# Kernel optimization log

Measured on AMD Instinct MI355X. Metric: run time of the kernel, lower is better.

The kernel has to match this reference:

```python
import jax, jax.numpy as jnp
import numpy as np

NEG_SLOPE = 0.01  # nn.LeakyReLU default


def setup_inputs() -> dict:
    key = jax.random.key(0)
    k1, k2, k3, k4, k5, k6 = jax.random.split(key, 6)
    N, E, F_IN, F_OUT = 50000, 800000, 256, 64
    x = jax.random.normal(k1, (N, F_IN), dtype=jnp.float32)
    src = jax.random.randint(k2, (E,), 0, N, dtype=jnp.int32)
    dst = jax.random.randint(k3, (E,), 0, N, dtype=jnp.int32)
    # nn.init.normal_(weight, 0, 0.5) for both Linear layers (no bias)
    W1 = 0.5 * jax.random.normal(k4, (F_OUT, F_IN), dtype=jnp.float32)
    W2 = 0.5 * jax.random.normal(k5, (F_OUT, F_OUT), dtype=jnp.float32)
    # detGAT.a = torch.rand(2*out_feats, 1)
    a = jax.random.uniform(k6, (2 * F_OUT, 1), dtype=jnp.float32)
    return {"x": x, "W1": W1, "W2": W2, "a": a, "src": src, "dst": dst}


def reference(x, W1, W2, a, src, dst):
    N, d = x.shape[0], W1.shape[0]
    # model_base: linear -> (dropout, identity in eval) -> relu, twice
    z = jax.nn.relu(x @ W1.T)
    h = jax.nn.relu(z @ W2.T)  # [N, d]
    # detGAT edge score: LeakyReLU(concat([h_dst, h_src]) @ a)
    # split a so we compute per-node dot products once instead of an [E, 2d] concat
    a_dst, a_src = a[:d, 0], a[d:, 0]
    s_dst = h @ a_dst  # [N]
    s_src = h @ a_src  # [N]
    score = jax.nn.leaky_relu(s_dst[dst] + s_src[src], NEG_SLOPE)  # [E]
    # edge_softmax: softmax over incoming edges of each destination node
    m = jax.ops.segment_max(score, dst, num_segments=N)  # [N]
    e = jnp.exp(score - m[dst])
    ssum = jax.ops.segment_sum(e, dst, num_segments=N)  # [N]
    w = e / ssum[dst]  # [E]
    # weighted scatter-sum of src features to dst nodes
    res = jax.ops.segment_sum(h[src] * w[:, None], dst, num_segments=N)  # [N, d]
    return jax.nn.relu(h - res)
```

## Files before the change

### kernel.cpp

```cpp
#include <hip/hip_runtime.h>
#include <math.h>

#define F_IN 256
#define F_OUT 64
#define NEG_SLOPE 0.01f
#define CAP 8192
#define NB2 256

typedef unsigned short ushort8_t __attribute__((ext_vector_type(8)));
typedef __bf16 bf16x8 __attribute__((ext_vector_type(8)));
typedef float f32x16 __attribute__((ext_vector_type(16)));

__device__ inline unsigned short f2bf(float f) {
    unsigned u = __float_as_uint(f);
    u += 0x7FFF + ((u >> 16) & 1);
    return (unsigned short)(u >> 16);
}
__device__ inline float bf2f(unsigned short u) {
    return __uint_as_float(((unsigned)u) << 16);
}
__device__ inline void splitbf(float x, unsigned short& hi, unsigned short& lo) {
    hi = f2bf(x);
    lo = f2bf(x - bf2f(hi));
}
__device__ inline bf16x8 asbf8(ushort8_t u) {
    union { ushort8_t u; bf16x8 b; } c; c.u = u; return c.b;
}
__device__ inline void split8u(const float4& p0, const float4& p1, ushort8_t& h, ushort8_t& l) {
    unsigned short th, tl;
    splitbf(p0.x, th, tl); h[0] = th; l[0] = tl;
    splitbf(p0.y, th, tl); h[1] = th; l[1] = tl;
    splitbf(p0.z, th, tl); h[2] = th; l[2] = tl;
    splitbf(p0.w, th, tl); h[3] = th; l[3] = tl;
    splitbf(p1.x, th, tl); h[4] = th; l[4] = tl;
    splitbf(p1.y, th, tl); h[5] = th; l[5] = tl;
    splitbf(p1.z, th, tl); h[6] = th; l[6] = tl;
    splitbf(p1.w, th, tl); h[7] = th; l[7] = tl;
}
__device__ inline float redq32(float v) {
    v += __shfl_xor(v, 1);  v += __shfl_xor(v, 2);  v += __shfl_xor(v, 4);
    v += __shfl_xor(v, 8);  v += __shfl_xor(v, 16);
    return v;
}

__global__ __launch_bounds__(1024)
void prep_scatter_kernel(const float* __restrict__ W1, const float* __restrict__ W2,
                         unsigned short* __restrict__ w1fh, unsigned short* __restrict__ w1fl,
                         unsigned short* __restrict__ w2fh, unsigned short* __restrict__ w2fl,
                         const float* __restrict__ x,
                         unsigned short* __restrict__ xfh, unsigned short* __restrict__ xfl,
                         int NTT, int N,
                         const int* __restrict__ src, const int* __restrict__ dst,
                         int* __restrict__ cursor, int* __restrict__ edata,
                         int E, int chunk)
{
    __shared__ int lh[256], lbase[256], lcur[256];
    const int tid = threadIdx.x;

    if (blockIdx.x < 16) {
        int idx = blockIdx.x * 1024 + tid;
        int jj = idx & 7, l = (idx >> 3) & 63, t = idx >> 9;
        {
            int nt = t & 1, gks = t >> 1;
            int f = nt * 32 + (l & 31);
            int k = gks * 16 + (l >> 5) * 8 + jj;
            unsigned short hi, lo;
            splitbf(W1[f * F_IN + k], hi, lo);
            w1fh[idx] = hi; w1fl[idx] = lo;
        }
        if (idx < 4096) {
            int nt = t & 1, ks = t >> 1;
            int f = nt * 32 + (l & 31);
            int j = ks * 16 + (l >> 5) * 8 + jj;
            unsigned short hi, lo;
            splitbf(W2[f * F_OUT + j], hi, lo);
            w2fh[idx] = hi; w2fl[idx] = lo;
        }
        return;
    }

    if (blockIdx.x < 16 + NTT) {
        const int t = blockIdx.x - 16;
        const int gks = tid >> 6, lane = tid & 63;
        const int ml = lane & 31, q = lane >> 5;
        const int row = min(t * 32 + ml, N - 1);
        const float* xr = x + (size_t)row * F_IN + gks * 16 + q * 8;
        float4 p0 = *(const float4*)xr;
        float4 p1 = *(const float4*)(xr + 4);
        ushort8_t h, l;
        split8u(p0, p1, h, l);
        size_t off = ((size_t)t * 1024 + tid) * 8;
        *(ushort8_t*)(xfh + off) = h;
        *(ushort8_t*)(xfl + off) = l;
        return;
    }

    const int bid = blockIdx.x - 16 - NTT;
    if (tid < 256) lh[tid] = 0;
    __syncthreads();
    const int beg = bid * chunk;
    const int end = min(E, beg + chunk);
    for (int i = beg + tid; i < end; i += 1024)
        atomicAdd(&lh[((unsigned)dst[i]) >> 8], 1);
    __syncthreads();
    if (tid < 256) {
        int c = lh[tid];
        lbase[tid] = c ? atomicAdd(&cursor[tid], c) : 0;
        lcur[tid] = 0;
    }
    __syncthreads();
    for (int i = beg + tid; i < end; i += 1024) {
        int d = dst[i];
        int s = src[i];
        int b = ((unsigned)d) >> 8;
        int rk = atomicAdd(&lcur[b], 1);
        edata[b * CAP + lbase[b] + rk] = ((d & 0xFF) << 16) | s;
    }
}

__global__ __launch_bounds__(256, 2)
void mlp_sort_kernel(const unsigned short* __restrict__ xfh,
                     const unsigned short* __restrict__ xfl,
                     const unsigned short* __restrict__ w1fh,
                     const unsigned short* __restrict__ w1fl,
                     const unsigned short* __restrict__ w2fh,
                     const unsigned short* __restrict__ w2fl,
                     const float* __restrict__ a,
                     unsigned short* __restrict__ hb,
                     float* __restrict__ sdst,
                     float* __restrict__ ssrc, int N,
                     const int* __restrict__ cursor,
                     const int* __restrict__ edata,
                     int* __restrict__ ssorted,
                     int* __restrict__ cnt, int* __restrict__ offs,
                     int MLPB)
{
    __shared__ __align__(16) unsigned short zbuf[4 * 4224];
    __shared__ int hist[256];
    __shared__ int excl[256];

    const int tid = threadIdx.x;
    const int lane = tid & 63;

    if (blockIdx.x < MLPB) {
        const int wid = __builtin_amdgcn_readfirstlane(tid >> 6);
        const int ml = lane & 31;
        const int q = lane >> 5;
        const int node0w = blockIdx.x * 128 + wid * 32;
        const int t = blockIdx.x * 4 + wid;

        unsigned short* zh = zbuf + wid * 4224;
        unsigned short* zl = zh + 2112;

        const unsigned short* __restrict__ xbh = xfh + (size_t)t * 8192;
        const unsigned short* __restrict__ xbl = xfl + (size_t)t * 8192;

        f32x16 acc0, acc1;
#pragma unroll
        for (int i = 0; i < 16; i++) { acc0[i] = 0.f; acc1[i] = 0.f; }

#pragma unroll
        for (int gks = 0; gks < 16; gks++) {
            bf16x8 ah = asbf8(*(const ushort8_t*)(xbh + gks * 512 + lane * 8));
            bf16x8 al = asbf8(*(const ushort8_t*)(xbl + gks * 512 + lane * 8));
            bf16x8 bh0 = asbf8(*(const ushort8_t*)(w1fh + ((gks * 2 + 0) * 64 + lane) * 8));
            bf16x8 bl0 = asbf8(*(const ushort8_t*)(w1fl + ((gks * 2 + 0) * 64 + lane) * 8));
            bf16x8 bh1 = asbf8(*(const ushort8_t*)(w1fh + ((gks * 2 + 1) * 64 + lane) * 8));
            bf16x8 bl1 = asbf8(*(const ushort8_t*)(w1fl + ((gks * 2 + 1) * 64 + lane) * 8));
            acc0 = __builtin_amdgcn_mfma_f32_32x32x16_bf16(ah, bh0, acc0, 0, 0, 0);
            acc0 = __builtin_amdgcn_mfma_f32_32x32x16_bf16(ah, bl0, acc0, 0, 0, 0);
            acc0 = __builtin_amdgcn_mfma_f32_32x32x16_bf16(al, bh0, acc0, 0, 0, 0);
            acc1 = __builtin_amdgcn_mfma_f32_32x32x16_bf16(ah, bh1, acc1, 0, 0, 0);
            acc1 = __builtin_amdgcn_mfma_f32_32x32x16_bf16(ah, bl1, acc1, 0, 0, 0);
            acc1 = __builtin_amdgcn_mfma_f32_32x32x16_bf16(al, bh1, acc1, 0, 0, 0);
        }

#pragma unroll
        for (int reg = 0; reg < 16; reg++) {
            int nd = (reg & 3) + 8 * (reg >> 2) + 4 * q;
            float z0 = fmaxf(acc0[reg], 0.f);
            float z1 = fmaxf(acc1[reg], 0.f);
            unsigned short h_, l_;
            splitbf(z0, h_, l_);
            zh[nd * 66 + ml] = h_; zl[nd * 66 + ml] = l_;
            splitbf(z1, h_, l_);
            zh[nd * 66 + 32 + ml] = h_; zl[nd * 66 + 32 + ml] = l_;
        }

        f32x16 hacc0, hacc1;
#pragma unroll
        for (int i = 0; i < 16; i++) { hacc0[i] = 0.f; hacc1[i] = 0.f; }
#pragma unroll
        for (int ks = 0; ks < 4; ks++) {
            bf16x8 wh0 = asbf8(*(const ushort8_t*)(w2fh + ((ks * 2 + 0) * 64 + lane) * 8));
            bf16x8 wl0 = asbf8(*(const ushort8_t*)(w2fl + ((ks * 2 + 0) * 64 + lane) * 8));
            bf16x8 wh1 = asbf8(*(const ushort8_t*)(w2fh + ((ks * 2 + 1) * 64 + lane) * 8));
            bf16x8 wl1 = asbf8(*(const ushort8_t*)(w2fl + ((ks * 2 + 1) * 64 + lane) * 8));
            bf16x8 ah = asbf8(*(const ushort8_t*)(zh + ml * 66 + ks * 16 + q * 8));
            bf16x8 al = asbf8(*(const ushort8_t*)(zl + ml * 66 + ks * 16 + q * 8));
            hacc0 = __builtin_amdgcn_mfma_f32_32x32x16_bf16(ah, wh0, hacc0, 0, 0, 0);
            hacc0 = __builtin_amdgcn_mfma_f32_32x32x16_bf16(ah, wl0, hacc0, 0, 0, 0);
            hacc0 = __builtin_amdgcn_mfma_f32_32x32x16_bf16(al, wh0, hacc0, 0, 0, 0);
            hacc1 = __builtin_amdgcn_mfma_f32_32x32x16_bf16(ah, wh1, hacc1, 0, 0, 0);
            hacc1 = __builtin_amdgcn_mfma_f32_32x32x16_bf16(ah, wl1, hacc1, 0, 0, 0);
            hacc1 = __builtin_amdgcn_mfma_f32_32x32x16_bf16(al, wh1, hacc1, 0, 0, 0);
        }

        const float aD0 = a[ml],            aD1 = a[32 + ml];
        const float aS0 = a[F_OUT + ml],    aS1 = a[F_OUT + 32 + ml];

        float sdv = 0.f, ssv = 0.f;
#pragma unroll
        for (int reg = 0; reg < 16; reg++) {
            int nd = (reg & 3) + 8 * (reg >> 2) + 4 * q;
            float h0 = fmaxf(hacc0[reg], 0.f);
            float h1 = fmaxf(hacc1[reg], 0.f);
            float td = redq32(h0 * aD0 + h1 * aD1);
            float ts = redq32(h0 * aS0 + h1 * aS1);
            if (ml == nd) { sdv = td; ssv = ts; }
            int gn = node0w + nd;
            if (gn < N) {
                hb[(size_t)gn * F_OUT + ml]      = f2bf(h0);
                hb[(size_t)gn * F_OUT + 32 + ml] = f2bf(h1);
            }
        }
        {
            int gn = node0w + ml;
            if ((((ml >> 2) & 1) == q) && gn < N) {
                sdst[gn] = sdv;
                ssrc[gn] = ssv;
            }
        }
        return;
    }

    const int cb = blockIdx.x - MLPB;
    const int base = cb * CAP;
    const int ecnt = cursor[cb];

    hist[tid] = 0;
    __syncthreads();
    for (int i = tid; i < ecnt; i += 256)
        atomicAdd(&hist[((unsigned)edata[base + i]) >> 16], 1);
    __syncthreads();

    if (tid < 64) {
        int v0 = hist[lane * 4], v1 = hist[lane * 4 + 1];
        int v2 = hist[lane * 4 + 2], v3 = hist[lane * 4 + 3];
        int ts = v0 + v1 + v2 + v3;
        int s = ts;
#pragma unroll
        for (int d = 1; d < 64; d <<= 1) {
            int t = __shfl_up(s, d);
            if (lane >= d) s += t;
        }
        int e = s - ts;
        excl[lane * 4] = e;
        excl[lane * 4 + 1] = e + v0;
        excl[lane * 4 + 2] = e + v0 + v1;
        excl[lane * 4 + 3] = e + v0 + v1 + v2;
    }
    __syncthreads();

    {
        int d = cb * 256 + tid;
        if (d < N) {
            cnt[d] = hist[tid];
            offs[d] = base + excl[tid];
        }
    }
    __syncthreads();

    for (int i = tid; i < ecnt; i += 256) {
        int pack = edata[base + i];
        int low = ((unsigned)pack) >> 16;
        int rk = atomicAdd(&excl[low], 1);
        ssorted[base + rk] = pack & 0xFFFF;
    }
}

__global__ __launch_bounds__(256)
void aggregate_kernel(const unsigned short* __restrict__ hb,
                      const float* __restrict__ sdst,
                      const float* __restrict__ ssrc,
                      const int* __restrict__ offs,
                      const int* __restrict__ cnt,
                      const int* __restrict__ ssorted,
                      float* __restrict__ out, int N)
{
    __shared__ float2 ws_sh[4][64];
    const int tid = threadIdx.x;
    const int lane = tid & 63;
    const int wid = tid >> 6;
    const int g = lane >> 4;
    const int li = lane & 15;
    const int d = blockIdx.x * 16 + wid * 4 + g;
    const bool vd = d < N;

    const int off = vd ? offs[d] : 0;
    const int deg = vd ? cnt[d] : 0;
    const float sdd = vd ? sdst[d] : 0.f;

    float M = -INFINITY, S = 0.f;
    float c0 = 0.f, c1 = 0.f, c2 = 0.f, c3 = 0.f;

    for (int cb = 0; cb < deg; cb += 16) {
        int ce = min(16, deg - cb);
        float score = -INFINITY;
        int s = 0;
        if (li < ce) {
            s = ssorted[off + cb + li];
            float sc = sdd + ssrc[s];
            score = sc > 0.f ? sc : NEG_SLOPE * sc;
        }
        float mc = score;
        mc = fmaxf(mc, __shfl_xor(mc, 1));
        mc = fmaxf(mc, __shfl_xor(mc, 2));
        mc = fmaxf(mc, __shfl_xor(mc, 4));
        mc = fmaxf(mc, __shfl_xor(mc, 8));
        float newM = fmaxf(M, mc);
        float scale = __expf(M - newM);
        float w = (li < ce) ? __expf(score - newM) : 0.f;
        ws_sh[wid][lane] = make_float2(w, __int_as_float(s));
        float csum = w;
        csum += __shfl_xor(csum, 1);
        csum += __shfl_xor(csum, 2);
        csum += __shfl_xor(csum, 4);
        csum += __shfl_xor(csum, 8);
        S = S * scale + csum;
        __builtin_amdgcn_wave_barrier();

        float t0 = 0.f, t1 = 0.f, t2 = 0.f, t3 = 0.f;
#pragma unroll
        for (int e = 0; e < 16; e++) {
            float2 tw = ws_sh[wid][g * 16 + e];
            int se = __float_as_int(tw.y);
            ushort4 r = *(const ushort4*)(hb + (((size_t)(unsigned)se) << 6) + li * 4);
            t0 = fmaf(tw.x, bf2f(r.x), t0);
            t1 = fmaf(tw.x, bf2f(r.y), t1);
            t2 = fmaf(tw.x, bf2f(r.z), t2);
            t3 = fmaf(tw.x, bf2f(r.w), t3);
        }
        c0 = c0 * scale + t0;
        c1 = c1 * scale + t1;
        c2 = c2 * scale + t2;
        c3 = c3 * scale + t3;
        __builtin_amdgcn_wave_barrier();
        M = newM;
    }

    if (vd) {
        ushort4 hr = *(const ushort4*)(hb + (((size_t)(unsigned)d) << 6) + li * 4);
        float inv = (S > 0.f) ? 1.f / S : 0.f;
        float r0 = bf2f(hr.x) - c0 * inv;
        float r1 = bf2f(hr.y) - c1 * inv;
        float r2 = bf2f(hr.z) - c2 * inv;
        float r3 = bf2f(hr.w) - c3 * inv;
        float4 o;
        o.x = r0 > 0.f ? r0 : 0.f;
        o.y = r1 > 0.f ? r1 : 0.f;
        o.z = r2 > 0.f ? r2 : 0.f;
        o.w = r3 > 0.f ? r3 : 0.f;
        *(float4*)(out + (size_t)d * F_OUT + li * 4) = o;
    }
}

extern "C" void kernel_launch(void* const* d_in, const int* in_sizes, int n_in,
                              void* d_out, int out_size, void* d_ws,
                              size_t ws_size, hipStream_t stream)
{
    const float* x  = (const float*)d_in[0];
    const float* W1 = (const float*)d_in[1];
    const float* W2 = (const float*)d_in[2];
    const float* a  = (const float*)d_in[3];
    const int* src  = (const int*)d_in[4];
    const int* dst  = (const int*)d_in[5];
    const int N = in_sizes[0] / F_IN;
    const int E = in_sizes[4];

    const int nbc = (N + 255) >> 8;
    const int MLPB = (N + 127) >> 7;
    const int NTT = MLPB * 4;
    const int chunk = (E + NB2 - 1) / NB2;

    float* ws = (float*)d_ws;
    float* sdst = ws;
    float* ssrc = sdst + N;
    unsigned short* w1fh = (unsigned short*)(ssrc + N);
    unsigned short* w1fl = w1fh + 16384;
    unsigned short* w2fh = w1fl + 16384;
    unsigned short* w2fl = w2fh + 4096;
    unsigned short* xfh = w2fl + 4096;
    unsigned short* xfl = xfh + (size_t)NTT * 8192;
    unsigned short* hb = xfl + (size_t)NTT * 8192;
    int* cnt    = (int*)(hb + (size_t)N * F_OUT);
    int* offs   = cnt + N;
    int* cursor = offs + N;
    int* edata  = cursor + 256;
    int* ssorted = edata + 196 * CAP;

    hipMemsetAsync(cursor, 0, 256 * sizeof(int), stream);
    prep_scatter_kernel<<<16 + NTT + NB2, 1024, 0, stream>>>(
        W1, W2, w1fh, w1fl, w2fh, w2fl,
        x, xfh, xfl, NTT, N,
        src, dst, cursor, edata, E, chunk);
    mlp_sort_kernel<<<MLPB + nbc, 256, 0, stream>>>(xfh, xfl, w1fh, w1fl, w2fh, w2fl, a,
                                                    hb, sdst, ssrc, N,
                                                    cursor, edata, ssorted, cnt, offs,
                                                    MLPB);
    aggregate_kernel<<<(N + 15) / 16, 256, 0, stream>>>(hb, sdst, ssrc, offs, cnt,
                                                        ssorted, (float*)d_out, N);
}
```

Before: 161.3 us.

## Fuse x bf16 hi/lo split into MLP kernel via LDS staging

Removes the separate pass that split x into bf16 hi/lo fragments in global memory. The MLP kernel now reads fp32 x directly, splits it in registers, and stages the result in a padded shared-memory tile before the MFMA loop. This avoids writing and re-reading about 51 MB of intermediate data. The cost is doubled LDS per block and split work sitting on the critical path of the MLP kernel, which may lower occupancy.

```diff
diff --git a/kernel.cpp b/kernel.cpp
--- a/kernel.cpp
+++ b/kernel.cpp
@@ -26,17 +26,6 @@
 __device__ inline bf16x8 asbf8(ushort8_t u) {
     union { ushort8_t u; bf16x8 b; } c; c.u = u; return c.b;
 }
-__device__ inline void split8u(const float4& p0, const float4& p1, ushort8_t& h, ushort8_t& l) {
-    unsigned short th, tl;
-    splitbf(p0.x, th, tl); h[0] = th; l[0] = tl;
-    splitbf(p0.y, th, tl); h[1] = th; l[1] = tl;
-    splitbf(p0.z, th, tl); h[2] = th; l[2] = tl;
-    splitbf(p0.w, th, tl); h[3] = th; l[3] = tl;
-    splitbf(p1.x, th, tl); h[4] = th; l[4] = tl;
-    splitbf(p1.y, th, tl); h[5] = th; l[5] = tl;
-    splitbf(p1.z, th, tl); h[6] = th; l[6] = tl;
-    splitbf(p1.w, th, tl); h[7] = th; l[7] = tl;
-}
 __device__ inline float redq32(float v) {
     v += __shfl_xor(v, 1);  v += __shfl_xor(v, 2);  v += __shfl_xor(v, 4);
     v += __shfl_xor(v, 8);  v += __shfl_xor(v, 16);
@@ -47,9 +36,6 @@
 void prep_scatter_kernel(const float* __restrict__ W1, const float* __restrict__ W2,
                          unsigned short* __restrict__ w1fh, unsigned short* __restrict__ w1fl,
                          unsigned short* __restrict__ w2fh, unsigned short* __restrict__ w2fl,
-                         const float* __restrict__ x,
-                         unsigned short* __restrict__ xfh, unsigned short* __restrict__ xfl,
-                         int NTT, int N,
                          const int* __restrict__ src, const int* __restrict__ dst,
                          int* __restrict__ cursor, int* __restrict__ edata,
                          int E, int chunk)
@@ -79,23 +65,7 @@
         return;
     }
 
-    if (blockIdx.x < 16 + NTT) {
-        const int t = blockIdx.x - 16;
-        const int gks = tid >> 6, lane = tid & 63;
-        const int ml = lane & 31, q = lane >> 5;
-        const int row = min(t * 32 + ml, N - 1);
-        const float* xr = x + (size_t)row * F_IN + gks * 16 + q * 8;
-        float4 p0 = *(const float4*)xr;
-        float4 p1 = *(const float4*)(xr + 4);
-        ushort8_t h, l;
-        split8u(p0, p1, h, l);
-        size_t off = ((size_t)t * 1024 + tid) * 8;
-        *(ushort8_t*)(xfh + off) = h;
-        *(ushort8_t*)(xfl + off) = l;
-        return;
-    }
-
-    const int bid = blockIdx.x - 16 - NTT;
+    const int bid = blockIdx.x - 16;
     if (tid < 256) lh[tid] = 0;
     __syncthreads();
     const int beg = bid * chunk;
@@ -119,8 +89,7 @@
 }
 
 __global__ __launch_bounds__(256, 2)
-void mlp_sort_kernel(const unsigned short* __restrict__ xfh,
-                     const unsigned short* __restrict__ xfl,
+void mlp_sort_kernel(const float* __restrict__ x,
                      const unsigned short* __restrict__ w1fh,
                      const unsigned short* __restrict__ w1fl,
                      const unsigned short* __restrict__ w2fh,
@@ -135,7 +104,7 @@
                      int* __restrict__ cnt, int* __restrict__ offs,
                      int MLPB)
 {
-    __shared__ __align__(16) unsigned short zbuf[4 * 4224];
+    __shared__ __align__(16) unsigned short zbuf[4 * 8576];
     __shared__ int hist[256];
     __shared__ int excl[256];
 
@@ -146,33 +115,56 @@
         const int wid = __builtin_amdgcn_readfirstlane(tid >> 6);
         const int ml = lane & 31;
         const int q = lane >> 5;
+        const int hl = lane >> 5;
+        const int cl = lane & 31;
         const int node0w = blockIdx.x * 128 + wid * 32;
-        const int t = blockIdx.x * 4 + wid;
-
-        unsigned short* zh = zbuf + wid * 4224;
-        unsigned short* zl = zh + 2112;
-
-        const unsigned short* __restrict__ xbh = xfh + (size_t)t * 8192;
-        const unsigned short* __restrict__ xbl = xfl + (size_t)t * 8192;
+
+        unsigned short* xh = zbuf + wid * 8576;
+        unsigned short* xl = xh + 4288;
+        unsigned short* zh = xh;
+        unsigned short* zl = xh + 2112;
 
         f32x16 acc0, acc1;
 #pragma unroll
         for (int i = 0; i < 16; i++) { acc0[i] = 0.f; acc1[i] = 0.f; }
 
 #pragma unroll
-        for (int gks = 0; gks < 16; gks++) {
-            bf16x8 ah = asbf8(*(const ushort8_t*)(xbh + gks * 512 + lane * 8));
-            bf16x8 al = asbf8(*(const ushort8_t*)(xbl + gks * 512 + lane * 8));
-            bf16x8 bh0 = asbf8(*(const ushort8_t*)(w1fh + ((gks * 2 + 0) * 64 + lane) * 8));
-            bf16x8 bl0 = asbf8(*(const ushort8_t*)(w1fl + ((gks * 2 + 0) * 64 + lane) * 8));
-            bf16x8 bh1 = asbf8(*(const ushort8_t*)(w1fh + ((gks * 2 + 1) * 64 + lane) * 8));
-            bf16x8 bl1 = asbf8(*(const ushort8_t*)(w1fl + ((gks * 2 + 1) * 64 + lane) * 8));
-            acc0 = __builtin_amdgcn_mfma_f32_32x32x16_bf16(ah, bh0, acc0, 0, 0, 0);
-            acc0 = __builtin_amdgcn_mfma_f32_32x32x16_bf16(ah, bl0, acc0, 0, 0, 0);
-            acc0 = __builtin_amdgcn_mfma_f32_32x32x16_bf16(al, bh0, acc0, 0, 0, 0);
-            acc1 = __builtin_amdgcn_mfma_f32_32x32x16_bf16(ah, bh1, acc1, 0, 0, 0);
-            acc1 = __builtin_amdgcn_mfma_f32_32x32x16_bf16(ah, bl1, acc1, 0, 0, 0);
-            acc1 = __builtin_amdgcn_mfma_f32_32x32x16_bf16(al, bh1, acc1, 0, 0, 0);
+        for (int half = 0; half < 2; half++) {
+            float4 v[16];
+#pragma unroll
+            for (int i = 0; i < 16; i++) {
+                int r = 2 * i + hl;
+                int rr = min(node0w + r, N - 1);
+                v[i] = *(const float4*)(x + (size_t)rr * F_IN + half * 128 + cl * 4);
+            }
+#pragma unroll
+            for (int i = 0; i < 16; i++) {
+                int r = 2 * i + hl;
+                ushort4 h4, l4;
+                unsigned short th, tl;
+                splitbf(v[i].x, th, tl); h4.x = th; l4.x = tl;
+                splitbf(v[i].y, th, tl); h4.y = th; l4.y = tl;
+                splitbf(v[i].z, th, tl); h4.z = th; l4.z = tl;
+                splitbf(v[i].w, th, tl); h4.w = th; l4.w = tl;
+                *(ushort4*)(xh + r * 134 + cl * 4) = h4;
+                *(ushort4*)(xl + r * 134 + cl * 4) = l4;
+            }
+#pragma unroll
+            for (int ks = 0; ks < 8; ks++) {
+                int gks = half * 8 + ks;
+                bf16x8 ah = asbf8(*(const ushort8_t*)(xh + ml * 134 + ks * 16 + q * 8));
+                bf16x8 al = asbf8(*(const ushort8_t*)(xl + ml * 134 + ks * 16 + q * 8));
+                bf16x8 bh0 = asbf8(*(const ushort8_t*)(w1fh + ((gks * 2 + 0) * 64 + lane) * 8));
+                bf16x8 bl0 = asbf8(*(const ushort8_t*)(w1fl + ((gks * 2 + 0) * 64 + lane) * 8));
+                bf16x8 bh1 = asbf8(*(const ushort8_t*)(w1fh + ((gks * 2 + 1) * 64 + lane) * 8));
+                bf16x8 bl1 = asbf8(*(const ushort8_t*)(w1fl + ((gks * 2 + 1) * 64 + lane) * 8));
+                acc0 = __builtin_amdgcn_mfma_f32_32x32x16_bf16(ah, bh0, acc0, 0, 0, 0);
+                acc0 = __builtin_amdgcn_mfma_f32_32x32x16_bf16(ah, bl0, acc0, 0, 0, 0);
+                acc0 = __builtin_amdgcn_mfma_f32_32x32x16_bf16(al, bh0, acc0, 0, 0, 0);
+                acc1 = __builtin_amdgcn_mfma_f32_32x32x16_bf16(ah, bh1, acc1, 0, 0, 0);
+                acc1 = __builtin_amdgcn_mfma_f32_32x32x16_bf16(ah, bl1, acc1, 0, 0, 0);
+                acc1 = __builtin_amdgcn_mfma_f32_32x32x16_bf16(al, bh1, acc1, 0, 0, 0);
+            }
         }
 
 #pragma unroll
@@ -378,11 +370,6 @@
     const int N = in_sizes[0] / F_IN;
     const int E = in_sizes[4];
 
-    const int nbc = (N + 255) >> 8;
-    const int MLPB = (N + 127) >> 7;
-    const int NTT = MLPB * 4;
-    const int chunk = (E + NB2 - 1) / NB2;
-
     float* ws = (float*)d_ws;
     float* sdst = ws;
     float* ssrc = sdst + N;
@@ -390,21 +377,21 @@
     unsigned short* w1fl = w1fh + 16384;
     unsigned short* w2fh = w1fl + 16384;
     unsigned short* w2fl = w2fh + 4096;
-    unsigned short* xfh = w2fl + 4096;
-    unsigned short* xfl = xfh + (size_t)NTT * 8192;
-    unsigned short* hb = xfl + (size_t)NTT * 8192;
+    unsigned short* hb = w2fl + 4096;
     int* cnt    = (int*)(hb + (size_t)N * F_OUT);
     int* offs   = cnt + N;
     int* cursor = offs + N;
     int* edata  = cursor + 256;
     int* ssorted = edata + 196 * CAP;
 
+    const int nbc = (N + 255) >> 8;
+    const int MLPB = (N + 127) >> 7;
+    const int chunk = (E + NB2 - 1) / NB2;
+
     hipMemsetAsync(cursor, 0, 256 * sizeof(int), stream);
-    prep_scatter_kernel<<<16 + NTT + NB2, 1024, 0, stream>>>(
-        W1, W2, w1fh, w1fl, w2fh, w2fl,
-        x, xfh, xfl, NTT, N,
-        src, dst, cursor, edata, E, chunk);
-    mlp_sort_kernel<<<MLPB + nbc, 256, 0, stream>>>(xfh, xfl, w1fh, w1fl, w2fh, w2fl, a,
+    prep_scatter_kernel<<<16 + NB2, 1024, 0, stream>>>(W1, W2, w1fh, w1fl, w2fh, w2fl,
+                                                       src, dst, cursor, edata, E, chunk);
+    mlp_sort_kernel<<<MLPB + nbc, 256, 0, stream>>>(x, w1fh, w1fl, w2fh, w2fl, a,
                                                     hb, sdst, ssrc, N,
                                                     cursor, edata, ssorted, cnt, offs,
                                                     MLPB);
```

Result: faster. 147.9 us (-8.3%).
